# Kernel tuning notes

Measured on AMD Instinct MI355X. Metric: run time of the kernel, lower is better.

The kernel has to match this reference:

```python
import jax, jax.numpy as jnp
import numpy as np

NOT_EPSILON = 1.0
B, K, Q, T = 2, 512, 512, 128


def swishmax(x, axis):
    # x * exp(x - max) normalized by sum(|.|) + 1 along `axis`
    xexp = x * jnp.exp(x - jnp.max(x, axis=axis, keepdims=True))
    return xexp / (jnp.sum(jnp.abs(xexp), axis=axis, keepdims=True) + NOT_EPSILON)


def setup_inputs() -> dict:
    key = jax.random.key(0)
    ks = jax.random.split(key, 8)
    scale = 1.0 / np.sqrt(T)
    return {
        "query_tokens": jax.random.normal(ks[0], (B, Q, T), dtype=jnp.float32),
        "key_tokens": jax.random.normal(ks[1], (B, K, T), dtype=jnp.float32),
        "value_tokens": jax.random.normal(ks[2], (B, K, T), dtype=jnp.float32),
        "Wk": jax.random.normal(ks[3], (T, T), dtype=jnp.float32) * scale,
        "Wq": jax.random.normal(ks[4], (T, T), dtype=jnp.float32) * scale,
        "Wv": jax.random.normal(ks[5], (T, T), dtype=jnp.float32) * scale,
        "Wl": jax.random.normal(ks[6], (T, T), dtype=jnp.float32) * scale,
        "Wo": jax.random.normal(ks[7], (T, T), dtype=jnp.float32) * scale,
    }


def reference(query_tokens, key_tokens, value_tokens, Wk, Wq, Wv, Wl, Wo):
    lin = lambda x, W: jnp.einsum('...t,ut->...u', x, W)  # nn.Linear(bias=False): x @ W.T
    k = lin(key_tokens, Wk)       # [B, K, T]
    q = lin(query_tokens, Wq)     # [B, Q, T]
    # outer-product broadcast over tokens: [B, K, Q, T]
    attention_raw = k[..., :, None, :] * q[..., None, :, :]
    attention_logits = lin(attention_raw, Wl)            # [B, K, Q, T]
    attention_scale = swishmax(attention_logits, axis=-2)  # normalize over Q (dim=-2)
    v = lin(value_tokens, Wv)     # [B, K, T]
    values_scaled = v[..., :, None, :] * attention_scale  # [B, K, Q, T]
    value_sum = values_scaled.sum(axis=-3)                # sum over K -> [B, Q, T]
    return lin(value_sum, Wo)
```

## Files before the change

kernel.cpp:

```cpp
#include <hip/hip_runtime.h>


using f16    = _Float16;
using f16x4  = __attribute__((ext_vector_type(4)))  f16;
using f16x8  = __attribute__((ext_vector_type(8)))  f16;
using f32x16 = __attribute__((ext_vector_type(16))) float;

#define LOG2E 1.4426950408889634f

__device__ __forceinline__ float exp2b(float x) {
  return __builtin_amdgcn_exp2f(x);
}

__device__ __forceinline__ f16x8 cvt8(float4 a, float4 b) {
  f16x8 r;
  r[0]=(f16)a.x; r[1]=(f16)a.y; r[2]=(f16)a.z; r[3]=(f16)a.w;
  r[4]=(f16)b.x; r[5]=(f16)b.y; r[6]=(f16)b.z; r[7]=(f16)b.w;
  return r;
}

__global__ __launch_bounds__(256, 2) void k1_proj(
    const float* __restrict__ q_tok, const float* __restrict__ k_tok,
    const float* __restrict__ v_tok, const float* __restrict__ Wq,
    const float* __restrict__ Wk,    const float* __restrict__ Wv,
    f16* __restrict__ qh, float* __restrict__ kls, float* __restrict__ vf)
{
  const int gid    = blockIdx.x;
  const int tensor = gid >> 4;
  const int sub    = gid & 15;
  const int b      = sub >> 3;
  const int rt     = sub & 7;
  const float* X = tensor==0 ? q_tok : (tensor==1 ? k_tok : v_tok);
  const float* W = tensor==0 ? Wq    : (tensor==1 ? Wk    : Wv);

  const int tid = threadIdx.x;
  const int w = tid >> 6, lane = tid & 63;
  const int l31 = lane & 31, lhi = lane >> 5;
  const int rbase = rt*64 + (w>>1)*32;
  const int cbase = (w&1)*64;

  f32x16 C0, C1;
  #pragma unroll
  for (int i=0;i<16;++i){ C0[i]=0.f; C1[i]=0.f; }

  #pragma unroll
  for (int kc=0; kc<8; ++kc) {
    const float* ap = X + (size_t)(b*512 + rbase + l31)*128 + kc*16 + 8*lhi;
    f16x8 a = cvt8(*(const float4*)ap, *(const float4*)(ap+4));
    const float* bp0 = W + (size_t)(cbase + l31)*128 + kc*16 + 8*lhi;
    f16x8 b0 = cvt8(*(const float4*)bp0, *(const float4*)(bp0+4));
    C0 = __builtin_amdgcn_mfma_f32_32x32x16_f16(a, b0, C0, 0, 0, 0);
    const float* bp1 = bp0 + 32*128;
    f16x8 b1 = cvt8(*(const float4*)bp1, *(const float4*)(bp1+4));
    C1 = __builtin_amdgcn_mfma_f32_32x32x16_f16(a, b1, C1, 0, 0, 0);
  }

  #pragma unroll
  for (int us=0; us<2; ++us) {
    #pragma unroll
    for (int r=0; r<16; ++r) {
      const int row = rbase + (r&3) + 8*(r>>2) + 4*lhi;
      const int col = cbase + us*32 + l31;
      const float val = us ? C1[r] : C0[r];
      const size_t idx = (size_t)(b*512 + row)*128 + col;
      if (tensor==0)      qh[idx]  = (f16)val;
      else if (tensor==1) kls[idx] = val * LOG2E;
      else                vf[idx]  = val;
    }
  }
}

__global__ __launch_bounds__(1024, 4) void k2_main(
    const f16* __restrict__ qh, const float* __restrict__ kls,
    const float* __restrict__ vf, const float* __restrict__ Wl,
    f16* __restrict__ part)
{
  const int gid  = blockIdx.x;
  const int b    = gid >> 7;
  const int uq   = (gid >> 5) & 3;
  const int grp  = gid & 31;
  const int kk0  = grp * 16;

  const int tid = threadIdx.x;
  const int w = tid >> 6, lane = tid & 63;
  const int l31 = lane & 31, lhi = lane >> 5;
  const int ubase = uq * 32;
  const int qbase = w * 32;

  __shared__ f16    Bl[2][32][136];
  __shared__ float2 red[2][16][32];

  f16x8 af[8];
  {
    const f16* ab = qh + (size_t)(b*512 + qbase + l31)*128 + 8*lhi;
    #pragma unroll
    for (int kc=0; kc<8; ++kc) af[kc] = *(const f16x8*)(ab + kc*16);
  }

  const int bu = tid >> 5;
  const int tc = tid & 31;
  const float4 wl = *(const float4*)(Wl + (size_t)(ubase + bu)*128 + tc*4);

  const float* kbase = kls + (size_t)(b*512 + kk0)*128 + tc*4;
  const float* vbase = vf  + (size_t)(b*512 + kk0)*128 + ubase;

  f32x16 acc;
  #pragma unroll
  for (int i=0;i<16;++i) acc[i]=0.f;

  {
    const float4 k0 = *(const float4*)(kbase);
    f16x4 o;
    o[0]=(f16)(wl.x*k0.x); o[1]=(f16)(wl.y*k0.y);
    o[2]=(f16)(wl.z*k0.z); o[3]=(f16)(wl.w*k0.w);
    *(f16x4*)(&Bl[0][bu][tc*4]) = o;
  }
  float4 n0 = *(const float4*)(kbase + 128);
  __syncthreads();

  for (int i=0; i<16; ++i) {
    const int cur = i & 1;

    const float v0 = vbase[i*128 + l31];

    if (i < 15) {
      f16x4 o;
      o[0]=(f16)(wl.x*n0.x); o[1]=(f16)(wl.y*n0.y);
      o[2]=(f16)(wl.z*n0.z); o[3]=(f16)(wl.w*n0.w);
      *(f16x4*)(&Bl[cur^1][bu][tc*4]) = o;
      if (i < 14) n0 = *(const float4*)(kbase + (i+2)*128);
    }

    f32x16 C;
    #pragma unroll
    for (int j=0;j<16;++j) C[j]=0.f;
    #pragma unroll
    for (int kc=0; kc<8; ++kc) {
      f16x8 bfr = *(const f16x8*)(&Bl[cur][l31][kc*16 + 8*lhi]);
      C = __builtin_amdgcn_mfma_f32_32x32x16_f16(af[kc], bfr, C, 0,0,0);
    }

    float mxa=-3.4e38f, mxb=-3.4e38f, sa=0.f, sb=0.f;
    #pragma unroll
    for (int r=0; r<16; ++r) {
      const float y = C[r];
      const float p = y * exp2b(y);
      C[r] = p;
      if (r & 1) { mxb = fmaxf(mxb, y); sb += fabsf(p); }
      else       { mxa = fmaxf(mxa, y); sa += fabsf(p); }
    }
    float mx = fmaxf(mxa, mxb);
    float sm = sa + sb;
    mx = fmaxf(mx, __shfl_xor(mx, 32));
    sm += __shfl_xor(sm, 32);
    if (lane < 32) red[cur][w][lane] = make_float2(mx, sm);

    __syncthreads();

    float M = -3.4e38f, S = 0.f;
    #pragma unroll
    for (int ww=0; ww<16; ++ww) {
      const float2 t = red[cur][ww][l31];
      M = fmaxf(M, t.x); S += t.y;
    }
    const float su = v0 / (S + LOG2E * exp2b(M));

    #pragma unroll
    for (int r=0; r<16; ++r)
      acc[r] = fmaf(su, C[r], acc[r]);

    __syncthreads();
  }

  {
    const int s = (grp<<3) + (b<<2) + uq;
    f16* pbase = part + (size_t)s*16384 + l31;
    #pragma unroll
    for (int r=0; r<16; ++r) {
      const int q = qbase + (r&3) + 8*(r>>2) + 4*lhi;
      pbase[q*32] = (f16)acc[r];
    }
  }
}

__global__ __launch_bounds__(256, 4) void k3a_reduce(
    const f16* __restrict__ part, f16* __restrict__ vsum16)
{
  const int fid = blockIdx.x*256 + threadIdx.x;
  const int u8 = fid & 15;
  const int q  = (fid >> 4) & 511;
  const int b  = fid >> 13;
  const int uq  = u8 >> 2;
  const int ul0 = (u8 & 3) * 8;

  float s[8];
  #pragma unroll
  for (int j=0;j<8;++j) s[j]=0.f;

  const f16* pb = part + (size_t)((b<<2) + uq)*16384 + q*32 + ul0;
  for (int g=0; g<32; ++g) {
    const f16x8 p = *(const f16x8*)(pb + (size_t)g*131072);
    #pragma unroll
    for (int j=0;j<8;++j) s[j] += (float)p[j];
  }

  f16x8 o;
  #pragma unroll
  for (int j=0;j<8;++j) o[j] = (f16)s[j];
  *(f16x8*)(vsum16 + ((size_t)(b*512 + q)*128 + u8*8)) = o;
}

__global__ __launch_bounds__(256, 2) void k3b_out(
    const f16* __restrict__ vsum16, const float* __restrict__ Wo,
    float* __restrict__ out)
{
  const int gid = blockIdx.x;
  const int qt = gid >> 1, b = gid & 1;
  const int rbase = qt * 32;
  const int tid = threadIdx.x;
  const int w = tid >> 6, lane = tid & 63;
  const int l31 = lane & 31, lhi = lane >> 5;
  const int cbase = w * 32;

  f32x16 C;
  #pragma unroll
  for (int i=0;i<16;++i) C[i] = 0.f;

  const f16* ab = vsum16 + (size_t)(b*512 + rbase + l31)*128 + 8*lhi;
  #pragma unroll
  for (int kc=0; kc<8; ++kc) {
    f16x8 a = *(const f16x8*)(ab + kc*16);
    const float* bp = Wo + (size_t)(cbase + l31)*128 + kc*16 + 8*lhi;
    f16x8 bfr = cvt8(*(const float4*)bp, *(const float4*)(bp+4));
    C = __builtin_amdgcn_mfma_f32_32x32x16_f16(a, bfr, C, 0, 0, 0);
  }

  #pragma unroll
  for (int r=0; r<16; ++r) {
    const int row = rbase + (r&3) + 8*(r>>2) + 4*lhi;
    const int col = cbase + l31;
    out[(size_t)(b*512 + row)*128 + col] = C[r];
  }
}

extern "C" void kernel_launch(void* const* d_in, const int* in_sizes, int n_in,
                              void* d_out, int out_size, void* d_ws, size_t ws_size,
                              hipStream_t stream) {
  const float* q_tok = (const float*)d_in[0];
  const float* k_tok = (const float*)d_in[1];
  const float* v_tok = (const float*)d_in[2];
  const float* Wk    = (const float*)d_in[3];
  const float* Wq    = (const float*)d_in[4];
  const float* Wv    = (const float*)d_in[5];
  const float* Wl    = (const float*)d_in[6];
  const float* Wo    = (const float*)d_in[7];

  char* ws = (char*)d_ws;
  f16*   qh     = (f16*)  (ws);
  float* kls    = (float*)(ws + 262144);
  float* vf     = (float*)(ws + 786432);
  f16*   part   = (f16*)  (ws + 1310720);
  f16*   vsum16 = (f16*)  (ws + 9699328);

  k1_proj<<<48, 256, 0, stream>>>(q_tok, k_tok, v_tok, Wq, Wk, Wv, qh, kls, vf);
  k2_main<<<256, 1024, 0, stream>>>(qh, kls, vf, Wl, part);
  k3a_reduce<<<64, 256, 0, stream>>>(part, vsum16);
  k3b_out<<<32, 256, 0, stream>>>(vsum16, Wo, (float*)d_out);
}
```

Baseline: 120.1 us.

## Process two keys per main-loop iteration and fuse partial reduction into output GEMM

The main kernel now handles two key rows per iteration, with double LDS B tiles and float4 reduction slots. This halves the number of block-wide barriers and cross-wave reduction rounds, and the two independent MFMA chains can interleave. The separate partial-sum reduction kernel is folded into the output projection kernel, which sums the 32 partials into shared memory before the MFMA, removing one launch and the intermediate buffer round trip. The costs are higher register and LDS pressure in the main kernel, and a reduction spread over only 32 blocks in the output kernel.

```diff
diff --git a/kernel.cpp b/kernel.cpp
--- a/kernel.cpp
+++ b/kernel.cpp
@@ -87,8 +87,8 @@
   const int ubase = uq * 32;
   const int qbase = w * 32;
 
-  __shared__ f16    Bl[2][32][136];
-  __shared__ float2 red[2][16][32];
+  __shared__ f16    Bl[2][2][32][136];
+  __shared__ float4 red[2][16][32];
 
   f16x8 af[8];
   {
@@ -109,65 +109,95 @@
   for (int i=0;i<16;++i) acc[i]=0.f;
 
   {
-    const float4 k0 = *(const float4*)(kbase);
-    f16x4 o;
-    o[0]=(f16)(wl.x*k0.x); o[1]=(f16)(wl.y*k0.y);
-    o[2]=(f16)(wl.z*k0.z); o[3]=(f16)(wl.w*k0.w);
-    *(f16x4*)(&Bl[0][bu][tc*4]) = o;
-  }
-  float4 n0 = *(const float4*)(kbase + 128);
+    const float4 ka = *(const float4*)(kbase);
+    const float4 kb = *(const float4*)(kbase + 128);
+    f16x4 oa, ob;
+    oa[0]=(f16)(wl.x*ka.x); oa[1]=(f16)(wl.y*ka.y);
+    oa[2]=(f16)(wl.z*ka.z); oa[3]=(f16)(wl.w*ka.w);
+    ob[0]=(f16)(wl.x*kb.x); ob[1]=(f16)(wl.y*kb.y);
+    ob[2]=(f16)(wl.z*kb.z); ob[3]=(f16)(wl.w*kb.w);
+    *(f16x4*)(&Bl[0][0][bu][tc*4]) = oa;
+    *(f16x4*)(&Bl[0][1][bu][tc*4]) = ob;
+  }
+  float4 na = *(const float4*)(kbase + 256);
+  float4 nb = *(const float4*)(kbase + 384);
   __syncthreads();
 
-  for (int i=0; i<16; ++i) {
+  for (int i=0; i<8; ++i) {
     const int cur = i & 1;
 
-    const float v0 = vbase[i*128 + l31];
-
-    if (i < 15) {
-      f16x4 o;
-      o[0]=(f16)(wl.x*n0.x); o[1]=(f16)(wl.y*n0.y);
-      o[2]=(f16)(wl.z*n0.z); o[3]=(f16)(wl.w*n0.w);
-      *(f16x4*)(&Bl[cur^1][bu][tc*4]) = o;
-      if (i < 14) n0 = *(const float4*)(kbase + (i+2)*128);
-    }
-
-    f32x16 C;
-    #pragma unroll
-    for (int j=0;j<16;++j) C[j]=0.f;
+    const float v0 = vbase[(2*i)*128   + l31];
+    const float v1 = vbase[(2*i+1)*128 + l31];
+
+    if (i < 7) {
+      f16x4 oa, ob;
+      oa[0]=(f16)(wl.x*na.x); oa[1]=(f16)(wl.y*na.y);
+      oa[2]=(f16)(wl.z*na.z); oa[3]=(f16)(wl.w*na.w);
+      ob[0]=(f16)(wl.x*nb.x); ob[1]=(f16)(wl.y*nb.y);
+      ob[2]=(f16)(wl.z*nb.z); ob[3]=(f16)(wl.w*nb.w);
+      *(f16x4*)(&Bl[cur^1][0][bu][tc*4]) = oa;
+      *(f16x4*)(&Bl[cur^1][1][bu][tc*4]) = ob;
+      if (i < 6) {
+        na = *(const float4*)(kbase + (2*i+4)*128);
+        nb = *(const float4*)(kbase + (2*i+5)*128);
+      }
+    }
+
+    f32x16 C0, C1;
+    #pragma unroll
+    for (int j=0;j<16;++j){ C0[j]=0.f; C1[j]=0.f; }
     #pragma unroll
     for (int kc=0; kc<8; ++kc) {
-      f16x8 bfr = *(const f16x8*)(&Bl[cur][l31][kc*16 + 8*lhi]);
-      C = __builtin_amdgcn_mfma_f32_32x32x16_f16(af[kc], bfr, C, 0,0,0);
-    }
-
-    float mxa=-3.4e38f, mxb=-3.4e38f, sa=0.f, sb=0.f;
-    #pragma unroll
-    for (int r=0; r<16; ++r) {
-      const float y = C[r];
-      const float p = y * exp2b(y);
-      C[r] = p;
-      if (r & 1) { mxb = fmaxf(mxb, y); sb += fabsf(p); }
-      else       { mxa = fmaxf(mxa, y); sa += fabsf(p); }
-    }
-    float mx = fmaxf(mxa, mxb);
-    float sm = sa + sb;
-    mx = fmaxf(mx, __shfl_xor(mx, 32));
-    sm += __shfl_xor(sm, 32);
-    if (lane < 32) red[cur][w][lane] = make_float2(mx, sm);
+      f16x8 b0 = *(const f16x8*)(&Bl[cur][0][l31][kc*16 + 8*lhi]);
+      f16x8 b1 = *(const f16x8*)(&Bl[cur][1][l31][kc*16 + 8*lhi]);
+      C0 = __builtin_amdgcn_mfma_f32_32x32x16_f16(af[kc], b0, C0, 0,0,0);
+      C1 = __builtin_amdgcn_mfma_f32_32x32x16_f16(af[kc], b1, C1, 0,0,0);
+    }
+
+    float mx0a=-3.4e38f, mx0b=-3.4e38f, s0a=0.f, s0b=0.f;
+    float mx1a=-3.4e38f, mx1b=-3.4e38f, s1a=0.f, s1b=0.f;
+    #pragma unroll
+    for (int r=0; r<16; ++r) {
+      const float y0 = C0[r], y1 = C1[r];
+      const float p0 = y0 * exp2b(y0);
+      const float p1 = y1 * exp2b(y1);
+      C0[r] = p0; C1[r] = p1;
+      if (r & 1) { mx0b=fmaxf(mx0b,y0); s0b+=fabsf(p0);
+                   mx1b=fmaxf(mx1b,y1); s1b+=fabsf(p1); }
+      else       { mx0a=fmaxf(mx0a,y0); s0a+=fabsf(p0);
+                   mx1a=fmaxf(mx1a,y1); s1a+=fabsf(p1); }
+    }
+    float mx0 = fmaxf(mx0a,mx0b), mx1 = fmaxf(mx1a,mx1b);
+    float sm0 = s0a+s0b,          sm1 = s1a+s1b;
+    mx0 = fmaxf(mx0, __shfl_xor(mx0, 32));
+    mx1 = fmaxf(mx1, __shfl_xor(mx1, 32));
+    sm0 += __shfl_xor(sm0, 32);
+    sm1 += __shfl_xor(sm1, 32);
+    if (lane < 32)
+      red[cur][w][lane] = make_float4(mx0, sm0, mx1, sm1);
 
     __syncthreads();
 
-    float M = -3.4e38f, S = 0.f;
-    #pragma unroll
-    for (int ww=0; ww<16; ++ww) {
-      const float2 t = red[cur][ww][l31];
-      M = fmaxf(M, t.x); S += t.y;
-    }
-    const float su = v0 / (S + LOG2E * exp2b(M));
-
-    #pragma unroll
-    for (int r=0; r<16; ++r)
-      acc[r] = fmaf(su, C[r], acc[r]);
+    float M0=-3.4e38f, S0=0.f, M1=-3.4e38f, S1=0.f;
+    #pragma unroll
+    for (int j=0; j<8; ++j) {
+      const float4 t = red[cur][8*lhi + j][l31];
+      M0 = fmaxf(M0, t.x); S0 += t.y;
+      M1 = fmaxf(M1, t.z); S1 += t.w;
+    }
+    M0 = fmaxf(M0, __shfl_xor(M0, 32));
+    S0 += __shfl_xor(S0, 32);
+    M1 = fmaxf(M1, __shfl_xor(M1, 32));
+    S1 += __shfl_xor(S1, 32);
+
+    const float su0 = v0 / (S0 + LOG2E * exp2b(M0));
+    const float su1 = v1 / (S1 + LOG2E * exp2b(M1));
+
+    #pragma unroll
+    for (int r=0; r<16; ++r) {
+      acc[r] = fmaf(su0, C0[r], acc[r]);
+      acc[r] = fmaf(su1, C1[r], acc[r]);
+    }
 
     __syncthreads();
   }
@@ -183,41 +213,42 @@
   }
 }
 
-__global__ __launch_bounds__(256, 4) void k3a_reduce(
-    const f16* __restrict__ part, f16* __restrict__ vsum16)
-{
-  const int fid = blockIdx.x*256 + threadIdx.x;
-  const int u8 = fid & 15;
-  const int q  = (fid >> 4) & 511;
-  const int b  = fid >> 13;
-  const int uq  = u8 >> 2;
-  const int ul0 = (u8 & 3) * 8;
-
-  float s[8];
-  #pragma unroll
-  for (int j=0;j<8;++j) s[j]=0.f;
-
-  const f16* pb = part + (size_t)((b<<2) + uq)*16384 + q*32 + ul0;
-  for (int g=0; g<32; ++g) {
-    const f16x8 p = *(const f16x8*)(pb + (size_t)g*131072);
-    #pragma unroll
-    for (int j=0;j<8;++j) s[j] += (float)p[j];
-  }
-
-  f16x8 o;
-  #pragma unroll
-  for (int j=0;j<8;++j) o[j] = (f16)s[j];
-  *(f16x8*)(vsum16 + ((size_t)(b*512 + q)*128 + u8*8)) = o;
-}
-
-__global__ __launch_bounds__(256, 2) void k3b_out(
-    const f16* __restrict__ vsum16, const float* __restrict__ Wo,
+__global__ __launch_bounds__(256, 2) void k3_out(
+    const f16* __restrict__ part, const float* __restrict__ Wo,
     float* __restrict__ out)
 {
   const int gid = blockIdx.x;
   const int qt = gid >> 1, b = gid & 1;
   const int rbase = qt * 32;
   const int tid = threadIdx.x;
+
+  __shared__ f16 vt[32][136];
+
+  {
+    const int q  = tid >> 3;
+    const int uc = tid & 7;
+    const int uq  = uc >> 1;
+    const int ul0 = (uc & 1) * 16;
+
+    float s[16];
+    #pragma unroll
+    for (int j=0;j<16;++j) s[j]=0.f;
+
+    const f16* pb = part + (size_t)((b<<2) + uq)*16384 + (rbase + q)*32 + ul0;
+    for (int g=0; g<32; ++g) {
+      const f16x8 p0 = *(const f16x8*)(pb + (size_t)g*131072);
+      const f16x8 p1 = *(const f16x8*)(pb + (size_t)g*131072 + 8);
+      #pragma unroll
+      for (int j=0;j<8;++j) { s[j] += (float)p0[j]; s[8+j] += (float)p1[j]; }
+    }
+    f16x8 o0, o1;
+    #pragma unroll
+    for (int j=0;j<8;++j) { o0[j] = (f16)s[j]; o1[j] = (f16)s[8+j]; }
+    *(f16x8*)(&vt[q][uc*16])     = o0;
+    *(f16x8*)(&vt[q][uc*16 + 8]) = o1;
+  }
+  __syncthreads();
+
   const int w = tid >> 6, lane = tid & 63;
   const int l31 = lane & 31, lhi = lane >> 5;
   const int cbase = w * 32;
@@ -226,10 +257,9 @@
   #pragma unroll
   for (int i=0;i<16;++i) C[i] = 0.f;
 
-  const f16* ab = vsum16 + (size_t)(b*512 + rbase + l31)*128 + 8*lhi;
   #pragma unroll
   for (int kc=0; kc<8; ++kc) {
-    f16x8 a = *(const f16x8*)(ab + kc*16);
+    f16x8 a = *(const f16x8*)(&vt[l31][kc*16 + 8*lhi]);
     const float* bp = Wo + (size_t)(cbase + l31)*128 + kc*16 + 8*lhi;
     f16x8 bfr = cvt8(*(const float4*)bp, *(const float4*)(bp+4));
     C = __builtin_amdgcn_mfma_f32_32x32x16_f16(a, bfr, C, 0, 0, 0);
@@ -256,14 +286,12 @@
   const float* Wo    = (const float*)d_in[7];
 
   char* ws = (char*)d_ws;
-  f16*   qh     = (f16*)  (ws);
-  float* kls    = (float*)(ws + 262144);
-  float* vf     = (float*)(ws + 786432);
-  f16*   part   = (f16*)  (ws + 1310720);
-  f16*   vsum16 = (f16*)  (ws + 9699328);
+  f16*   qh   = (f16*)  (ws);
+  float* kls  = (float*)(ws + 262144);
+  float* vf   = (float*)(ws + 786432);
+  f16*   part = (f16*)  (ws + 1310720);
 
   k1_proj<<<48, 256, 0, stream>>>(q_tok, k_tok, v_tok, Wq, Wk, Wv, qh, kls, vf);
   k2_main<<<256, 1024, 0, stream>>>(qh, kls, vf, Wl, part);
-  k3a_reduce<<<64, 256, 0, stream>>>(part, vsum16);
-  k3b_out<<<32, 256, 0, stream>>>(vsum16, Wo, (float*)d_out);
-}
+  k3_out<<<32, 256, 0, stream>>>(part, Wo, (float*)d_out);
+}
```

Measured after the change: 115.6 us. 1.04x faster.
